# Optimization experiments

Measured on AMD Instinct MI355X. Metric: run time of the kernel, lower is better.

Reference implementation:

```python
import jax, jax.numpy as jnp
import numpy as np

EPS = 1e-5


def batchnorm(x, gamma, beta):
    # training-mode BN over (N, T, V) per channel, biased variance (matches torch BN forward)
    mean = x.mean(axis=(0, 2, 3), keepdims=True)
    var = x.var(axis=(0, 2, 3), keepdims=True)
    return (x - mean) * jax.lax.rsqrt(var + EPS) * gamma[None, :, None, None] + beta[None, :, None, None]


def temporal_shift(x, shift, stride):
    # Per-channel learnable fractional temporal shift with linear interpolation,
    # zero padding outside [0, T) (reconstruction of Shift-GCN's CUDA shift op).
    N, C, T, V = x.shape
    Tout = T // stride
    pos = jnp.arange(Tout, dtype=x.dtype)[None, :] * stride + shift[:, None]  # (C, Tout)
    i0 = jnp.floor(pos).astype(jnp.int32)
    frac = pos - i0.astype(x.dtype)
    i1 = i0 + 1
    w0 = ((i0 >= 0) & (i0 < T)).astype(x.dtype) * (1.0 - frac)  # (C, Tout)
    w1 = ((i1 >= 0) & (i1 < T)).astype(x.dtype) * frac
    i0c = jnp.clip(i0, 0, T - 1)
    i1c = jnp.clip(i1, 0, T - 1)
    cidx = jnp.arange(C)[:, None]
    x0 = x[:, cidx, i0c]  # (N, C, Tout, V) gather along time per channel
    x1 = x[:, cidx, i1c]
    return x0 * w0[None, :, :, None] + x1 * w1[None, :, :, None]


def setup_inputs() -> dict:
    key = jax.random.key(0)
    ks = jax.random.split(key, 10)
    N, C, T, V = 64, 128, 300, 25
    D = 256  # out_channels
    R = C // 4  # SE reduction
    inp = {
        "x": jax.random.normal(ks[0], (N, C, T, V), dtype=jnp.float32),
        "epoch": 100,
        "bn1_gamma": jnp.ones((C,), jnp.float32),
        "bn1_beta": jnp.zeros((C,), jnp.float32),
        "bn2_gamma": jnp.ones((D,), jnp.float32),
        "bn2_beta": jnp.zeros((D,), jnp.float32),
        "shift_in_param": jax.random.uniform(ks[1], (C,), jnp.float32, -1.0, 1.0),
        "shift_out_param": jax.random.uniform(ks[2], (D,), jnp.float32, -1.0, 1.0),
        "fc1_w": jax.random.normal(ks[3], (R, C), jnp.float32) * (1.0 / np.sqrt(C)),
        "fc1_b": jnp.zeros((R,), jnp.float32),
        "fc2_w": jax.random.normal(ks[4], (4, R), jnp.float32) * (1.0 / np.sqrt(R)),
        "fc2_b": jnp.zeros((4,), jnp.float32),
        "temporal_weight": jax.random.normal(ks[5], (4, C, D), jnp.float32) * np.sqrt(1.0 / D),
        "temporal_bias": jnp.zeros((4, D), jnp.float32),
    }
    return inp


def reference(x, epoch, bn1_gamma, bn1_beta, bn2_gamma, bn2_beta,
              shift_in_param, shift_out_param, fc1_w, fc1_b, fc2_w, fc2_b,
              temporal_weight, temporal_bias):
    x = batchnorm(x, bn1_gamma, bn1_beta)
    x = temporal_shift(x, shift_in_param, 1)
    # DY_SEModule: global avg pool -> 1x1 convs -> temperature softmax gate over 4 branches
    p = x.mean(axis=(2, 3))  # (N, C)
    h = jax.nn.relu(p @ fc1_w.T + fc1_b)
    logits = h @ fc2_w.T + fc2_b  # (N, 4)
    tao = (-(30.0 - 1.0) / 60.0 * epoch + 30.0) if epoch < 60 else 1.0
    gate = jax.nn.softmax(logits / tao, axis=1)  # (N, 4)
    w = jnp.einsum('kcd,nk->ncd', temporal_weight, gate)  # per-sample dynamic weight
    b = jnp.einsum('kc,nk->nc', temporal_bias, gate)
    x = jnp.einsum('nctv,ncd->ndtv', x, w) + b[:, :, None, None]
    x = jax.nn.relu(x)
    x = temporal_shift(x, shift_out_param, 1)  # stride=1
    x = batchnorm(x, bn2_gamma, bn2_beta)
    return x
```

## Files before the change

### kernel.cpp

```cpp
#include <hip/hip_runtime.h>
#include <stdint.h>

#define NN 64
#define CC 128
#define TT 300
#define VV 25
#define TV 7500
#define DD 256
#define RR 32
#define JPAD 7552
#define JT 125
#define NJT 60
#define XSTR4 184
#define XROWB (XSTR4 * 4)
#define CBL 32

#define OFF_S1P    0
#define OFF_SS1P   8192
#define OFF_PS     16384
#define OFF_A1     24576
#define OFF_B1     24704
#define OFF_SUM2   24832
#define OFF_SUMSQ2 25088
#define OFF_A2     25344
#define OFF_B2     25600
#define OFF_GATE   25856
#define OFF_BIAS2  26112
#define OFF_CORR0  42496
#define OFF_CORR9  58880
#define FLOAT_REGION 75264
#define ZERO_CNT   25344
#define WT_BYTE_OFF ((size_t)FLOAT_REGION * 4)
#define WT_BYTES    ((size_t)NN * DD * CC * 2)
#define Z_BYTE_OFF  (WT_BYTE_OFF + WT_BYTES)

typedef __attribute__((ext_vector_type(8))) short short8;
typedef __attribute__((ext_vector_type(4))) float f32x4;

typedef const __attribute__((address_space(1))) uint32_t gas_u32;
typedef __attribute__((address_space(3))) uint32_t las_u32;

__device__ inline ushort f2bf(float f) {
    uint32_t u = __float_as_uint(f);
    u += 0x7fffu + ((u >> 16) & 1u);
    return (ushort)(u >> 16);
}
__device__ inline float bf2f(ushort v) { return __uint_as_float(((uint32_t)v) << 16); }
__device__ inline void async_copy16(const void* g, void* l) {
    __builtin_amdgcn_global_load_lds((gas_u32*)g, (las_u32*)l, 16, 0, 0);
}

__device__ inline void block_reduce2(float& a, float& b) {
    __shared__ float sa[4], sb[4];
    for (int off = 32; off > 0; off >>= 1) {
        a += __shfl_down(a, off);
        b += __shfl_down(b, off);
    }
    int lane = threadIdx.x & 63, wid = threadIdx.x >> 6;
    if (lane == 0) { sa[wid] = a; sb[wid] = b; }
    __syncthreads();
    if (threadIdx.x == 0) {
        a = sa[0] + sa[1] + sa[2] + sa[3];
        b = sb[0] + sb[1] + sb[2] + sb[3];
    }
}

__global__ void k_zero(float* ws) {
    int i = blockIdx.x * 256 + threadIdx.x;
    for (; i < ZERO_CNT; i += 32 * 256) ws[i] = 0.f;
}

__global__ __launch_bounds__(256) void k_shift_stats(const float* __restrict__ x,
                                                     const float* __restrict__ shift_in,
                                                     float* __restrict__ ws,
                                                     ushort* __restrict__ yT) {
    __shared__ float  xw[CBL * XSTR4];
    __shared__ ushort ytile[CBL * 128];
    int jt = blockIdx.x, ch = blockIdx.y, n = blockIdx.z;
    int j0 = jt * JT;
    int t0 = jt * 5;
    int t_lo = max(t0 - 1, 0);
    int start_f = (t_lo * VV) & ~3;
    int doff = t_lo * VV - start_f;
    int tid = threadIdx.x;
    int lane = tid & 63, w = tid >> 6;
    int nvalid = min(45, (TV - start_f) >> 2);

    const float* xbase = x + ((size_t)n * CC + ch * CBL) * TV;
#pragma unroll
    for (int rr = 0; rr < 8; ++rr) {
        int cl = w * 8 + rr;
        if (lane < nvalid)
            async_copy16((const char*)(xbase + (size_t)cl * TV + start_f) + lane * 16,
                         (char*)xw + cl * XROWB + lane * 16);
    }
    __syncthreads();

    int jq = tid & 7;
    int cl = tid >> 3;
    {
        int c = ch * CBL + cl;
        float sh = shift_in[c];
        bool posi = (sh >= 0.f);
        const float* xrow = &xw[cl * XSTR4];
        float s_p = 0.f, s_x = 0.f, s_xx = 0.f;
        int key = (cl & 7) ^ ((cl >> 3) & 7);
        for (int p = 0; p < 2; ++p) {
            int jb = p * 64 + jq * 8;
            ushort pk[8];
#pragma unroll
            for (int e = 0; e < 8; ++e) {
                int jtl = jb + e;
                float yv = 0.f, xv = 0.f;
                if (jtl < JT) {
                    int j = j0 + jtl;
                    int t = j / VV;
                    int v = j - t * VV;
                    float posf = (float)t + sh;
                    float f0 = floorf(posf);
                    int i0 = (int)f0;
                    float frac = posf - f0;
                    int i1 = i0 + 1;
                    float w0 = (i0 >= 0 && i0 < TT) ? (1.f - frac) : 0.f;
                    float w1 = (i1 >= 0 && i1 < TT) ? frac : 0.f;
                    int i0c = min(max(i0, 0), TT - 1), i1c = min(max(i1, 0), TT - 1);
                    float x0 = xrow[(i0c - t_lo) * VV + v + doff];
                    float x1 = xrow[(i1c - t_lo) * VV + v + doff];
                    yv = w0 * x0 + w1 * x1;
                    xv = posi ? x0 : x1;
                }
                s_p += yv; s_x += xv; s_xx += xv * xv;
                pk[e] = f2bf(yv);
            }
            uint32_t dw[4];
#pragma unroll
            for (int h = 0; h < 4; ++h) dw[h] = (uint32_t)pk[2 * h] | ((uint32_t)pk[2 * h + 1] << 16);
            int m = p * 8 + (jq ^ key);
            *(uint4*)&ytile[cl * 128 + m * 8] = *(uint4*)dw;
        }
        for (int off = 4; off > 0; off >>= 1) {
            s_p += __shfl_down(s_p, off, 8);
            s_x += __shfl_down(s_x, off, 8);
            s_xx += __shfl_down(s_xx, off, 8);
        }
        if (jq == 0) {
            atomicAdd(&ws[OFF_PS + n * CC + c], s_p);
            atomicAdd(&ws[OFF_S1P + c * 64 + n], s_x);
            atomicAdd(&ws[OFF_SS1P + c * 64 + n], s_xx);
        }
    }
    __syncthreads();

    for (int it = 0; it < 2; ++it) {
        int idx = it * 256 + tid;
        int s = idx & 3;
        int jl = idx >> 2;
        if (jl < JT) {
            int p = jl >> 6, jqv = (jl >> 3) & 7, e = jl & 7;
            uint32_t dw[4];
#pragma unroll
            for (int h = 0; h < 4; ++h) {
                int c0 = 8 * s + 2 * h, c1 = c0 + 1;
                int m0 = p * 8 + (jqv ^ (c0 & 7) ^ s);
                int m1 = p * 8 + (jqv ^ (c1 & 7) ^ s);
                ushort lo = ytile[c0 * 128 + m0 * 8 + e];
                ushort hi = ytile[c1 * 128 + m1 * 8 + e];
                dw[h] = (uint32_t)lo | ((uint32_t)hi << 16);
            }
            int jg = j0 + jl;
            int sg = ch * 4 + s;
            size_t rowb = ((size_t)n * JPAD + jg) * 128;
            *(uint4*)&yT[rowb + (size_t)((sg ^ (jg & 7)) << 3)] = *(uint4*)dw;
        }
    }
}

__global__ void k_bn1_final(const float* __restrict__ g1, const float* __restrict__ b1, float* ws) {
    int c = threadIdx.x;
    if (c < CC) {
        float s = 0.f, ss = 0.f;
        for (int g = 0; g < 64; ++g) { s += ws[OFF_S1P + c * 64 + g]; ss += ws[OFF_SS1P + c * 64 + g]; }
        const float inv = 1.f / (float)(NN * TV);
        float m = s * inv;
        float var = ss * inv - m * m;
        float rstd = rsqrtf(var + 1e-5f);
        float A = rstd * g1[c];
        ws[OFF_A1 + c] = A;
        ws[OFF_B1 + c] = b1[c] - m * A;
    }
}

__global__ void k_gate(const float* __restrict__ fc1_w, const float* __restrict__ fc1_b,
                       const float* __restrict__ fc2_w, const float* __restrict__ fc2_b,
                       const float* __restrict__ shift_in,
                       const int* __restrict__ epoch_p, float* ws) {
    __shared__ float psh[NN][CC];
    __shared__ float hsh[NN][RR];
    int tid = threadIdx.x;
    const float invTV = 1.f / (float)TV;
    for (int idx = tid; idx < NN * CC; idx += 256) {
        int n = idx >> 7, c = idx & 127;
        float sh = shift_in[c];
        float gb = (sh >= 0.f) ? (1.f - sh) : (1.f + sh);
        float meang = (299.f + gb) * (1.f / 300.f);
        psh[n][c] = ws[OFF_A1 + c] * (ws[OFF_PS + n * CC + c] * invTV) + ws[OFF_B1 + c] * meang;
    }
    __syncthreads();
    int n = tid >> 2;
    int rq = tid & 3;
    for (int r = rq * 8; r < rq * 8 + 8; ++r) {
        float acc = fc1_b[r];
        for (int c = 0; c < CC; ++c) acc += psh[n][c] * fc1_w[r * CC + c];
        hsh[n][r] = fmaxf(acc, 0.f);
    }
    __syncthreads();
    if (tid < NN) {
        int nn = tid;
        int ep = *epoch_p;
        float tao = (ep < 60) ? (-(29.f / 60.f) * (float)ep + 30.f) : 1.f;
        float li[4];
        float mx = -1e30f;
        for (int k = 0; k < 4; ++k) {
            float acc = fc2_b[k];
            for (int r = 0; r < RR; ++r) acc += hsh[nn][r] * fc2_w[k * RR + r];
            li[k] = acc / tao;
            mx = fmaxf(mx, li[k]);
        }
        float se = 0.f;
        for (int k = 0; k < 4; ++k) { li[k] = expf(li[k] - mx); se += li[k]; }
        float inv = 1.f / se;
        for (int k = 0; k < 4; ++k) ws[OFF_GATE + nn * 4 + k] = li[k] * inv;
    }
}

__global__ __launch_bounds__(256) void k_wmix(const float* __restrict__ tw, const float* __restrict__ tb,
                                              const float* __restrict__ shift_in,
                                              float* __restrict__ ws, ushort* __restrict__ wT) {
    int n = blockIdx.x, d = threadIdx.x;
    const float* g = &ws[OFF_GATE + n * 4];
    float g0 = g[0], g1 = g[1], g2 = g[2], g3 = g[3];
    float bias2 = g0 * tb[d] + g1 * tb[DD + d] + g2 * tb[2 * DD + d] + g3 * tb[3 * DD + d];
    float c0acc = 0.f, c9acc = 0.f;
    ushort* wrow = wT + ((size_t)n * DD + d) * 128;
    for (int s = 0; s < 16; ++s) {
        uint32_t dw[4];
#pragma unroll
        for (int h = 0; h < 4; ++h) {
            ushort e01[2];
#pragma unroll
            for (int q = 0; q < 2; ++q) {
                int c = s * 8 + 2 * h + q;
                const float* twc = tw + (size_t)c * DD + d;
                float wv = g0 * twc[0] + g1 * twc[32768] + g2 * twc[65536] + g3 * twc[98304];
                float A = ws[OFF_A1 + c], B = ws[OFF_B1 + c];
                float sh = shift_in[c];
                bias2 += B * wv;
                if (sh >= 0.f) c9acc += B * sh * wv; else c0acc += B * (-sh) * wv;
                e01[q] = f2bf(A * wv);
            }
            dw[h] = (uint32_t)e01[0] | ((uint32_t)e01[1] << 16);
        }
        *(uint4*)&wrow[(s ^ (d & 7)) << 3] = *(uint4*)dw;
    }
    ws[OFF_BIAS2 + n * DD + d] = bias2;
    ws[OFF_CORR0 + n * DD + d] = c0acc;
    ws[OFF_CORR9 + n * DD + d] = c9acc;
}

__global__ __launch_bounds__(256) void k_gemm(const ushort* __restrict__ yT,
                                              const ushort* __restrict__ wT,
                                              const float* __restrict__ ws,
                                              ushort* __restrict__ zbuf) {
    __shared__ ushort yl[128 * 128];
    __shared__ ushort wl[2][64 * 128];
    int jt = blockIdx.x, n = blockIdx.y;
    int tid = threadIdx.x;
    const char* ysrc = (const char*)(yT + ((size_t)n * JPAD + jt * 128) * 128);
    const char* wsrc = (const char*)(wT + (size_t)n * DD * 128);
#pragma unroll
    for (int i = 0; i < 8; ++i)
        async_copy16(ysrc + (size_t)(i * 256 + tid) * 16, (char*)yl + (i * 256 + tid) * 16);
#pragma unroll
    for (int i = 0; i < 4; ++i)
        async_copy16(wsrc + (size_t)(i * 256 + tid) * 16, (char*)wl[0] + (i * 256 + tid) * 16);
    __syncthreads();
    int lane = tid & 63, wid = tid >> 6;
    int wm = wid >> 1, wn = wid & 1;
    int l16 = lane & 15, g = lane >> 4;
    bool edge = (jt == 0) || (jt == 58);
#pragma unroll
    for (int dt = 0; dt < 4; ++dt) {
        if (dt < 3) {
            const char* wc = wsrc + (size_t)(dt + 1) * 16384;
#pragma unroll
            for (int i = 0; i < 4; ++i)
                async_copy16(wc + (size_t)(i * 256 + tid) * 16,
                             (char*)wl[(dt + 1) & 1] + (i * 256 + tid) * 16);
        }
        const ushort* wcur = wl[dt & 1];
        f32x4 acc[2][4];
#pragma unroll
        for (int a = 0; a < 2; ++a)
#pragma unroll
            for (int b = 0; b < 4; ++b) acc[a][b] = (f32x4)0.f;
#pragma unroll
        for (int ks = 0; ks < 4; ++ks) {
            short8 af[2], bfr[4];
            int chunk = (ks * 4 + g) ^ (l16 & 7);
#pragma unroll
            for (int mi = 0; mi < 2; ++mi)
                af[mi] = *(const short8*)&wcur[(wm * 32 + mi * 16 + l16) * 128 + chunk * 8];
#pragma unroll
            for (int ni = 0; ni < 4; ++ni)
                bfr[ni] = *(const short8*)&yl[(wn * 64 + ni * 16 + l16) * 128 + chunk * 8];
#pragma unroll
            for (int mi = 0; mi < 2; ++mi)
#pragma unroll
                for (int ni = 0; ni < 4; ++ni)
                    acc[mi][ni] = __builtin_amdgcn_mfma_f32_16x16x32_bf16(af[mi], bfr[ni], acc[mi][ni], 0, 0, 0);
        }
#pragma unroll
        for (int mi = 0; mi < 2; ++mi) {
#pragma unroll
            for (int r = 0; r < 4; ++r) {
                int d = dt * 64 + wm * 32 + mi * 16 + g * 4 + r;
                float bias = ws[OFF_BIAS2 + n * DD + d];
                float cr0 = 0.f, cr9 = 0.f;
                if (edge) { cr0 = ws[OFF_CORR0 + n * DD + d]; cr9 = ws[OFF_CORR9 + n * DD + d]; }
                size_t zrow = ((size_t)n * DD + d) * JPAD + jt * 128;
#pragma unroll
                for (int ni = 0; ni < 4; ++ni) {
                    int jl = wn * 64 + ni * 16 + l16;
                    float pre = acc[mi][ni][r] + bias;
                    if (edge) {
                        int jg = jt * 128 + jl;
                        if (jg < VV) pre -= cr0;
                        if (jg >= TV - VV) pre -= cr9;
                    }
                    zbuf[zrow + jl] = f2bf(fmaxf(pre, 0.f));
                }
            }
        }
        __syncthreads();
    }
}

__global__ __launch_bounds__(256) void k_bn2_stats(const ushort* __restrict__ zbuf,
                                                   const float* __restrict__ shift_out,
                                                   float* __restrict__ ws) {
    __shared__ ushort zl[JPAD];
    int d = blockIdx.x & 255;
    int n = blockIdx.x >> 8;
    int tid = threadIdx.x;
    const char* zrow = (const char*)(zbuf + ((size_t)n * DD + d) * JPAD);
    for (int k = tid; k < JPAD / 8; k += 256)
        async_copy16(zrow + (size_t)k * 16, (char*)zl + k * 16);
    __syncthreads();
    float sh = shift_out[d];
    float alpha = (sh >= 0.f) ? (1.f - sh) : (-sh);
    float beta  = (sh >= 0.f) ? sh : (1.f + sh);
    int o25 = (sh >= 0.f) ? 0 : -25;
    float s = 0.f, ss = 0.f;
    for (int jj = tid; jj < TV; jj += 256) {
        int i0 = jj + o25, i1 = jj + o25 + 25;
        float z0 = bf2f(zl[max(i0, 0)]);
        float z1 = bf2f(zl[min(i1, TV - 1)]);
        z0 = (i0 >= 0) ? z0 : 0.f;
        z1 = (i1 < TV) ? z1 : 0.f;
        float zs = alpha * z0 + beta * z1;
        s += zs;
        ss += zs * zs;
    }
    block_reduce2(s, ss);
    if (tid == 0) {
        atomicAdd(&ws[OFF_SUM2 + d], s);
        atomicAdd(&ws[OFF_SUMSQ2 + d], ss);
    }
}

__global__ void k_bn2_final(const float* __restrict__ g2, const float* __restrict__ b2, float* ws) {
    int d = threadIdx.x;
    if (d < DD) {
        const float inv = 1.f / (float)(NN * TV);
        float m = ws[OFF_SUM2 + d] * inv;
        float var = ws[OFF_SUMSQ2 + d] * inv - m * m;
        float rstd = rsqrtf(var + 1e-5f);
        float A = rstd * g2[d];
        ws[OFF_A2 + d] = A;
        ws[OFF_B2 + d] = b2[d] - m * A;
    }
}

__global__ __launch_bounds__(256) void k_out(const ushort* __restrict__ zbuf,
                                             const float* __restrict__ shift_out,
                                             const float* __restrict__ ws,
                                             float* __restrict__ out) {
    __shared__ ushort zl[JPAD];
    int d = blockIdx.x & 255;
    int n = blockIdx.x >> 8;
    int tid = threadIdx.x;
    const char* zrow = (const char*)(zbuf + ((size_t)n * DD + d) * JPAD);
    for (int k = tid; k < JPAD / 8; k += 256)
        async_copy16(zrow + (size_t)k * 16, (char*)zl + k * 16);
    __syncthreads();
    float sh = shift_out[d];
    float alpha = (sh >= 0.f) ? (1.f - sh) : (-sh);
    float beta  = (sh >= 0.f) ? sh : (1.f + sh);
    int o25 = (sh >= 0.f) ? 0 : -25;
    float A = ws[OFF_A2 + d], B = ws[OFF_B2 + d];
    float4* orow = (float4*)(out + ((size_t)n * DD + d) * TV);
    for (int k = tid; k < TV / 4; k += 256) {
        int jj = k * 4;
        float4 o4;
        float* op = &o4.x;
#pragma unroll
        for (int q = 0; q < 4; ++q) {
            int i0 = jj + q + o25, i1 = jj + q + o25 + 25;
            float z0 = bf2f(zl[max(i0, 0)]);
            float z1 = bf2f(zl[min(i1, TV - 1)]);
            z0 = (i0 >= 0) ? z0 : 0.f;
            z1 = (i1 < TV) ? z1 : 0.f;
            op[q] = (alpha * z0 + beta * z1) * A + B;
        }
        orow[k] = o4;
    }
}

extern "C" void kernel_launch(void* const* d_in, const int* in_sizes, int n_in,
                              void* d_out, int out_size, void* d_ws, size_t ws_size,
                              hipStream_t stream) {
    const float* x        = (const float*)d_in[0];
    const int*   epoch    = (const int*)d_in[1];
    const float* bn1_g    = (const float*)d_in[2];
    const float* bn1_b    = (const float*)d_in[3];
    const float* bn2_g    = (const float*)d_in[4];
    const float* bn2_b    = (const float*)d_in[5];
    const float* shift_in = (const float*)d_in[6];
    const float* shift_out= (const float*)d_in[7];
    const float* fc1_w    = (const float*)d_in[8];
    const float* fc1_b    = (const float*)d_in[9];
    const float* fc2_w    = (const float*)d_in[10];
    const float* fc2_b    = (const float*)d_in[11];
    const float* tw       = (const float*)d_in[12];
    const float* tb       = (const float*)d_in[13];
    float* out = (float*)d_out;
    float* ws  = (float*)d_ws;
    ushort* yT = (ushort*)d_out;
    ushort* wT = (ushort*)((char*)d_ws + WT_BYTE_OFF);
    ushort* zb = (ushort*)((char*)d_ws + Z_BYTE_OFF);

    k_zero<<<32, 256, 0, stream>>>(ws);
    k_shift_stats<<<dim3(NJT, 4, NN), 256, 0, stream>>>(x, shift_in, ws, yT);
    k_bn1_final<<<1, 128, 0, stream>>>(bn1_g, bn1_b, ws);
    k_gate<<<1, 256, 0, stream>>>(fc1_w, fc1_b, fc2_w, fc2_b, shift_in, epoch, ws);
    k_wmix<<<64, 256, 0, stream>>>(tw, tb, shift_in, ws, wT);
    k_gemm<<<dim3(59, 64), 256, 0, stream>>>(yT, wT, ws, zb);
    k_bn2_stats<<<16384, 256, 0, stream>>>(zb, shift_out, ws);
    k_bn2_final<<<1, 256, 0, stream>>>(bn2_g, bn2_b, ws);
    k_out<<<16384, 256, 0, stream>>>(zb, shift_out, ws, out);
}
```

Baseline: 507.8 us.

## Stage GEMM output through LDS for coalesced stores, hoist B fragments, fold tiny kernels

The GEMM epilogue now writes bf16 results into an LDS staging tile and then stores them to global memory as 16-byte coalesced rows, replacing the scattered 2-byte stores. Y-operand fragments are loaded once into registers before the d-tile loop, so the Y tile's LDS is freed for reuse as the staging buffer, and launch_bounds asks for 2 blocks per CU. The bn1_final and bn2_final kernels are merged into k_gate and k_out to remove two launches. In exchange, register pressure rises from the 16 held fragments and extra barriers are added per d-tile.

```diff
diff --git a/kernel.cpp b/kernel.cpp
--- a/kernel.cpp
+++ b/kernel.cpp
@@ -14,6 +14,7 @@
 #define XSTR4 184
 #define XROWB (XSTR4 * 4)
 #define CBL 32
+#define ZSTR 136
 
 #define OFF_S1P    0
 #define OFF_SS1P   8192
@@ -22,8 +23,6 @@
 #define OFF_B1     24704
 #define OFF_SUM2   24832
 #define OFF_SUMSQ2 25088
-#define OFF_A2     25344
-#define OFF_B2     25600
 #define OFF_GATE   25856
 #define OFF_BIAS2  26112
 #define OFF_CORR0  42496
@@ -175,9 +174,16 @@
     }
 }
 
-__global__ void k_bn1_final(const float* __restrict__ g1, const float* __restrict__ b1, float* ws) {
-    int c = threadIdx.x;
-    if (c < CC) {
+__global__ void k_gate(const float* __restrict__ g1, const float* __restrict__ b1,
+                       const float* __restrict__ fc1_w, const float* __restrict__ fc1_b,
+                       const float* __restrict__ fc2_w, const float* __restrict__ fc2_b,
+                       const float* __restrict__ shift_in,
+                       const int* __restrict__ epoch_p, float* ws) {
+    __shared__ float psh[NN][CC];
+    __shared__ float hsh[NN][RR];
+    int tid = threadIdx.x;
+    if (tid < CC) {
+        int c = tid;
         float s = 0.f, ss = 0.f;
         for (int g = 0; g < 64; ++g) { s += ws[OFF_S1P + c * 64 + g]; ss += ws[OFF_SS1P + c * 64 + g]; }
         const float inv = 1.f / (float)(NN * TV);
@@ -188,15 +194,7 @@
         ws[OFF_A1 + c] = A;
         ws[OFF_B1 + c] = b1[c] - m * A;
     }
-}
-
-__global__ void k_gate(const float* __restrict__ fc1_w, const float* __restrict__ fc1_b,
-                       const float* __restrict__ fc2_w, const float* __restrict__ fc2_b,
-                       const float* __restrict__ shift_in,
-                       const int* __restrict__ epoch_p, float* ws) {
-    __shared__ float psh[NN][CC];
-    __shared__ float hsh[NN][RR];
-    int tid = threadIdx.x;
+    __syncthreads();
     const float invTV = 1.f / (float)TV;
     for (int idx = tid; idx < NN * CC; idx += 256) {
         int n = idx >> 7, c = idx & 127;
@@ -267,12 +265,14 @@
     ws[OFF_CORR9 + n * DD + d] = c9acc;
 }
 
-__global__ __launch_bounds__(256) void k_gemm(const ushort* __restrict__ yT,
-                                              const ushort* __restrict__ wT,
-                                              const float* __restrict__ ws,
-                                              ushort* __restrict__ zbuf) {
-    __shared__ ushort yl[128 * 128];
-    __shared__ ushort wl[2][64 * 128];
+__global__ __launch_bounds__(256, 2) void k_gemm(const ushort* __restrict__ yT,
+                                                 const ushort* __restrict__ wT,
+                                                 const float* __restrict__ ws,
+                                                 ushort* __restrict__ zbuf) {
+    __shared__ char smem[65536];
+    ushort* yl  = (ushort*)smem;
+    ushort* zst = (ushort*)smem;
+    ushort* wlb[2] = { (ushort*)(smem + 32768), (ushort*)(smem + 49152) };
     int jt = blockIdx.x, n = blockIdx.y;
     int tid = threadIdx.x;
     const char* ysrc = (const char*)(yT + ((size_t)n * JPAD + jt * 128) * 128);
@@ -282,12 +282,21 @@
         async_copy16(ysrc + (size_t)(i * 256 + tid) * 16, (char*)yl + (i * 256 + tid) * 16);
 #pragma unroll
     for (int i = 0; i < 4; ++i)
-        async_copy16(wsrc + (size_t)(i * 256 + tid) * 16, (char*)wl[0] + (i * 256 + tid) * 16);
+        async_copy16(wsrc + (size_t)(i * 256 + tid) * 16, (char*)wlb[0] + (i * 256 + tid) * 16);
     __syncthreads();
     int lane = tid & 63, wid = tid >> 6;
     int wm = wid >> 1, wn = wid & 1;
     int l16 = lane & 15, g = lane >> 4;
     bool edge = (jt == 0) || (jt == 58);
+    short8 bfr[4][4];
+#pragma unroll
+    for (int ni = 0; ni < 4; ++ni)
+#pragma unroll
+        for (int ks = 0; ks < 4; ++ks) {
+            int chunk = (ks * 4 + g) ^ (l16 & 7);
+            bfr[ni][ks] = *(const short8*)&yl[(wn * 64 + ni * 16 + l16) * 128 + chunk * 8];
+        }
+    __syncthreads();
 #pragma unroll
     for (int dt = 0; dt < 4; ++dt) {
         if (dt < 3) {
@@ -295,9 +304,9 @@
 #pragma unroll
             for (int i = 0; i < 4; ++i)
                 async_copy16(wc + (size_t)(i * 256 + tid) * 16,
-                             (char*)wl[(dt + 1) & 1] + (i * 256 + tid) * 16);
-        }
-        const ushort* wcur = wl[dt & 1];
+                             (char*)wlb[(dt + 1) & 1] + (i * 256 + tid) * 16);
+        }
+        const ushort* wcur = wlb[dt & 1];
         f32x4 acc[2][4];
 #pragma unroll
         for (int a = 0; a < 2; ++a)
@@ -305,29 +314,26 @@
             for (int b = 0; b < 4; ++b) acc[a][b] = (f32x4)0.f;
 #pragma unroll
         for (int ks = 0; ks < 4; ++ks) {
-            short8 af[2], bfr[4];
+            short8 af[2];
             int chunk = (ks * 4 + g) ^ (l16 & 7);
 #pragma unroll
             for (int mi = 0; mi < 2; ++mi)
                 af[mi] = *(const short8*)&wcur[(wm * 32 + mi * 16 + l16) * 128 + chunk * 8];
 #pragma unroll
-            for (int ni = 0; ni < 4; ++ni)
-                bfr[ni] = *(const short8*)&yl[(wn * 64 + ni * 16 + l16) * 128 + chunk * 8];
-#pragma unroll
             for (int mi = 0; mi < 2; ++mi)
 #pragma unroll
                 for (int ni = 0; ni < 4; ++ni)
-                    acc[mi][ni] = __builtin_amdgcn_mfma_f32_16x16x32_bf16(af[mi], bfr[ni], acc[mi][ni], 0, 0, 0);
+                    acc[mi][ni] = __builtin_amdgcn_mfma_f32_16x16x32_bf16(af[mi], bfr[ni][ks], acc[mi][ni], 0, 0, 0);
         }
 #pragma unroll
         for (int mi = 0; mi < 2; ++mi) {
 #pragma unroll
             for (int r = 0; r < 4; ++r) {
-                int d = dt * 64 + wm * 32 + mi * 16 + g * 4 + r;
+                int dl = wm * 32 + mi * 16 + g * 4 + r;
+                int d = dt * 64 + dl;
                 float bias = ws[OFF_BIAS2 + n * DD + d];
                 float cr0 = 0.f, cr9 = 0.f;
                 if (edge) { cr0 = ws[OFF_CORR0 + n * DD + d]; cr9 = ws[OFF_CORR9 + n * DD + d]; }
-                size_t zrow = ((size_t)n * DD + d) * JPAD + jt * 128;
 #pragma unroll
                 for (int ni = 0; ni < 4; ++ni) {
                     int jl = wn * 64 + ni * 16 + l16;
@@ -337,9 +343,17 @@
                         if (jg < VV) pre -= cr0;
                         if (jg >= TV - VV) pre -= cr9;
                     }
-                    zbuf[zrow + jl] = f2bf(fmaxf(pre, 0.f));
+                    zst[dl * ZSTR + jl] = f2bf(fmaxf(pre, 0.f));
                 }
             }
+        }
+        __syncthreads();
+#pragma unroll
+        for (int it = 0; it < 4; ++it) {
+            int idx = it * 256 + tid;
+            int row = idx >> 4, q = idx & 15;
+            uint4 v = *(const uint4*)&zst[row * ZSTR + q * 8];
+            *(uint4*)&zbuf[((size_t)n * DD + dt * 64 + row) * JPAD + jt * 128 + q * 8] = v;
         }
         __syncthreads();
     }
@@ -378,21 +392,10 @@
     }
 }
 
-__global__ void k_bn2_final(const float* __restrict__ g2, const float* __restrict__ b2, float* ws) {
-    int d = threadIdx.x;
-    if (d < DD) {
-        const float inv = 1.f / (float)(NN * TV);
-        float m = ws[OFF_SUM2 + d] * inv;
-        float var = ws[OFF_SUMSQ2 + d] * inv - m * m;
-        float rstd = rsqrtf(var + 1e-5f);
-        float A = rstd * g2[d];
-        ws[OFF_A2 + d] = A;
-        ws[OFF_B2 + d] = b2[d] - m * A;
-    }
-}
-
 __global__ __launch_bounds__(256) void k_out(const ushort* __restrict__ zbuf,
                                              const float* __restrict__ shift_out,
+                                             const float* __restrict__ g2,
+                                             const float* __restrict__ b2,
                                              const float* __restrict__ ws,
                                              float* __restrict__ out) {
     __shared__ ushort zl[JPAD];
@@ -402,12 +405,17 @@
     const char* zrow = (const char*)(zbuf + ((size_t)n * DD + d) * JPAD);
     for (int k = tid; k < JPAD / 8; k += 256)
         async_copy16(zrow + (size_t)k * 16, (char*)zl + k * 16);
+    const float inv = 1.f / (float)(NN * TV);
+    float m = ws[OFF_SUM2 + d] * inv;
+    float var = ws[OFF_SUMSQ2 + d] * inv - m * m;
+    float rstd = rsqrtf(var + 1e-5f);
+    float A = rstd * g2[d];
+    float B = b2[d] - m * A;
     __syncthreads();
     float sh = shift_out[d];
     float alpha = (sh >= 0.f) ? (1.f - sh) : (-sh);
     float beta  = (sh >= 0.f) ? sh : (1.f + sh);
     int o25 = (sh >= 0.f) ? 0 : -25;
-    float A = ws[OFF_A2 + d], B = ws[OFF_B2 + d];
     float4* orow = (float4*)(out + ((size_t)n * DD + d) * TV);
     for (int k = tid; k < TV / 4; k += 256) {
         int jj = k * 4;
@@ -451,11 +459,9 @@
 
     k_zero<<<32, 256, 0, stream>>>(ws);
     k_shift_stats<<<dim3(NJT, 4, NN), 256, 0, stream>>>(x, shift_in, ws, yT);
-    k_bn1_final<<<1, 128, 0, stream>>>(bn1_g, bn1_b, ws);
-    k_gate<<<1, 256, 0, stream>>>(fc1_w, fc1_b, fc2_w, fc2_b, shift_in, epoch, ws);
+    k_gate<<<1, 256, 0, stream>>>(bn1_g, bn1_b, fc1_w, fc1_b, fc2_w, fc2_b, shift_in, epoch, ws);
     k_wmix<<<64, 256, 0, stream>>>(tw, tb, shift_in, ws, wT);
     k_gemm<<<dim3(59, 64), 256, 0, stream>>>(yT, wT, ws, zb);
     k_bn2_stats<<<16384, 256, 0, stream>>>(zb, shift_out, ws);
-    k_bn2_final<<<1, 256, 0, stream>>>(bn2_g, bn2_b, ws);
-    k_out<<<16384, 256, 0, stream>>>(zb, shift_out, ws, out);
-}
+    k_out<<<16384, 256, 0, stream>>>(zb, shift_out, bn2_g, bn2_b, ws, out);
+}
```

Result: faster. 487.0 us (-4.1%).
